# Performance work log

Measured on AMD Instinct MI355X. Metric: run time of the kernel, lower is better.

The kernel has to match this reference:

```python
import jax, jax.numpy as jnp
import numpy as np

IN, H, T = 40, 64, 301


def setup_inputs() -> dict:
    key = jax.random.key(0)
    ks = jax.random.split(key, 7)
    s_ih = 1.0 / np.sqrt(H)
    return {
        "x": jax.random.normal(ks[0], (4096, T, IN), dtype=jnp.float32),
        # PyTorch LSTM layout: gates stacked as [i, f, g, o] along first dim
        "w_ih": jax.random.uniform(ks[1], (4 * H, IN), jnp.float32, -s_ih, s_ih),
        "w_hh": jax.random.uniform(ks[2], (4 * H, H), jnp.float32, -s_ih, s_ih),
        "b_ih": jax.random.uniform(ks[3], (4 * H,), jnp.float32, -s_ih, s_ih),
        "b_hh": jax.random.uniform(ks[4], (4 * H,), jnp.float32, -s_ih, s_ih),
        "w_clf": jax.random.uniform(ks[5], (1, T * H), jnp.float32, -1.0 / np.sqrt(T * H), 1.0 / np.sqrt(T * H)),
        "b_clf": jax.random.uniform(ks[6], (1,), jnp.float32, -1.0 / np.sqrt(T * H), 1.0 / np.sqrt(T * H)),
    }


def _lstm(x, w_ih, w_hh, b_ih, b_hh):
    B = x.shape[0]
    # precompute input projections for all timesteps: [B, T, 4H] -> [T, B, 4H]
    xw = jnp.einsum("bti,gi->btg", x, w_ih) + b_ih + b_hh
    xw = jnp.transpose(xw, (1, 0, 2))

    def step(carry, xt):
        h, c = carry
        z = xt + h @ w_hh.T  # [B, 4H]
        i, f, g, o = jnp.split(z, 4, axis=-1)
        c = jax.nn.sigmoid(f) * c + jax.nn.sigmoid(i) * jnp.tanh(g)
        h = jax.nn.sigmoid(o) * jnp.tanh(c)
        return (h, c), h

    h0 = jnp.zeros((B, H), x.dtype)
    c0 = jnp.zeros((B, H), x.dtype)
    _, hs = jax.lax.scan(step, (h0, c0), xw)  # hs: [T, B, H]
    return jnp.transpose(hs, (1, 0, 2))  # [B, T, H]


def reference(x, w_ih, w_hh, b_ih, b_hh, w_clf, b_clf):
    out = _lstm(x, w_ih, w_hh, b_ih, b_hh)  # [B, T, H]
    flat = out.reshape(out.shape[0], -1)  # [B, T*H]
    return flat @ w_clf.T + b_clf  # [B, 1]
```

## Files before the change

kernel.cpp:

```cpp
#include <hip/hip_runtime.h>

#define T_STEPS 301
#define IN_DIM  40
#define LOG2E   1.44269504088896340736f

typedef __attribute__((ext_vector_type(8))) _Float16 f16x8;
typedef __attribute__((ext_vector_type(4))) float f32x4;
typedef unsigned short ushort_t;
typedef unsigned int uint_t;

union u16cv { _Float16 hf; ushort_t u; };

#define MFMA16(A, B, C) __builtin_amdgcn_mfma_f32_16x16x32_f16((A), (B), (C), 0, 0, 0)

__device__ __forceinline__ f16x8 cvt8h(const float4 a, const float4 b) {
  f16x8 r;
  r[0] = (_Float16)a.x; r[1] = (_Float16)a.y; r[2] = (_Float16)a.z; r[3] = (_Float16)a.w;
  r[4] = (_Float16)b.x; r[5] = (_Float16)b.y; r[6] = (_Float16)b.z; r[7] = (_Float16)b.w;
  return r;
}

__device__ __forceinline__ float lstm_act(float zi, float zf, float zg, float zo, float& cc) {
  const float ig = __builtin_amdgcn_rcpf(1.0f + __builtin_amdgcn_exp2f(-zi));
  const float fg = __builtin_amdgcn_rcpf(1.0f + __builtin_amdgcn_exp2f(-zf));
  const float gg = 1.0f - 2.0f * __builtin_amdgcn_rcpf(1.0f + __builtin_amdgcn_exp2f(zg));
  const float og = __builtin_amdgcn_rcpf(1.0f + __builtin_amdgcn_exp2f(-zo));
  cc = fg * cc + ig * gg;
  const float tc = 1.0f - 2.0f * __builtin_amdgcn_rcpf(1.0f + __builtin_amdgcn_exp2f(cc * (2.0f * LOG2E)));
  return og * tc;
}

__global__ __launch_bounds__(256, 1)
void lstm_fm(const float* __restrict__ x, const float* __restrict__ w_ih,
             const float* __restrict__ w_hh, const float* __restrict__ b_ih,
             const float* __restrict__ b_hh, const float* __restrict__ w_clf,
             const float* __restrict__ b_clf, float* __restrict__ out) {
  extern __shared__ char smem[];
  float*    wclf  = (float*)smem;
  ushort_t* hflat = (ushort_t*)(smem + 77056);
  float*    red   = (float*)(smem + 77056 + 4096);

  const int tid = threadIdx.x;
  const int l   = tid & 63, w = tid >> 6;
  const int c15 = l & 15, g16 = l >> 4;
  const int n   = w * 16 + c15;
  const int b0  = blockIdx.x * 16;
  const float gsc[4] = {LOG2E, LOG2E, 2.0f * LOG2E, LOG2E};

  for (int i = tid; i < (T_STEPS * 64) / 4; i += 256)
    ((float4*)wclf)[i] = ((const float4*)w_clf)[i];
  for (int i = tid; i < 1024; i += 256) ((uint_t*)hflat)[i] = 0;

  f16x8 whh[4][2], wih[4][2];
#pragma unroll
  for (int g = 0; g < 4; ++g) {
    const float s = gsc[g];
    const float* wr = w_hh + (size_t)(g * 64 + n) * 64;
#pragma unroll
    for (int kc = 0; kc < 2; ++kc) {
      float4 v0 = *(const float4*)(wr + kc * 32 + g16 * 8);
      float4 v1 = *(const float4*)(wr + kc * 32 + g16 * 8 + 4);
      v0.x *= s; v0.y *= s; v0.z *= s; v0.w *= s;
      v1.x *= s; v1.y *= s; v1.z *= s; v1.w *= s;
      whh[g][kc] = cvt8h(v0, v1);
    }
    const float* wi = w_ih + (size_t)(g * 64 + n) * IN_DIM;
    {
      float4 v0 = *(const float4*)(wi + g16 * 8);
      float4 v1 = *(const float4*)(wi + g16 * 8 + 4);
      v0.x *= s; v0.y *= s; v0.z *= s; v0.w *= s;
      v1.x *= s; v1.y *= s; v1.z *= s; v1.w *= s;
      wih[g][0] = cvt8h(v0, v1);
    }
    {
      float4 u0 = make_float4(0, 0, 0, 0), u1 = make_float4(0, 0, 0, 0);
      if (g16 == 0) {
        u0 = *(const float4*)(wi + 32);
        u1 = *(const float4*)(wi + 36);
        u0.x *= s; u0.y *= s; u0.z *= s; u0.w *= s;
        u1.x *= s; u1.y *= s; u1.z *= s; u1.w *= s;
      } else if (g16 == 1) {
        u0.x = (b_ih[g * 64 + n] + b_hh[g * 64 + n]) * s;
      }
      wih[g][1] = cvt8h(u0, u1);
    }
  }
  __syncthreads();

  const int akey = (c15 >> 2) << 4;
  const int ridx0 = c15 * 64 + ((0 * 32 + 8 * g16) ^ akey);
  const int ridx1 = c15 * 64 + ((1 * 32 + 8 * g16) ^ akey);
  int widx[4];
#pragma unroll
  for (int r = 0; r < 4; ++r) widx[r] = (4 * g16 + r) * 64 + (n ^ (g16 << 4));

  const float* xb = x + (size_t)(b0 + c15) * T_STEPS * IN_DIM;
  float4 px0 = *(const float4*)(xb + g16 * 8);
  float4 px1 = *(const float4*)(xb + g16 * 8 + 4);
  float4 pq0 = make_float4(0, 0, 0, 0), pq1 = make_float4(0, 0, 0, 0);
  if (g16 == 0) {
    pq0 = *(const float4*)(xb + 32);
    pq1 = *(const float4*)(xb + 36);
  }
  f16x8 xf1c = {};
  if (g16 == 1) xf1c[0] = (_Float16)1.0f;

  f32x4 z[4];
  float cc[4]  = {0.f, 0.f, 0.f, 0.f};
  float acl[4] = {0.f, 0.f, 0.f, 0.f};

  for (int t = 0; t < T_STEPS; ++t) {
    const int rb = (t & 1) * 1024, wb = 1024 - rb;

    f16x8 a0 = *(const f16x8*)(hflat + rb + ridx0);
    f16x8 a1 = *(const f16x8*)(hflat + rb + ridx1);

    f16x8 xf0 = cvt8h(px0, px1);
    f16x8 xf1 = xf1c;
    if (g16 == 0) xf1 = cvt8h(pq0, pq1);
#pragma unroll
    for (int g = 0; g < 4; ++g) {
      f32x4 zz = {0.f, 0.f, 0.f, 0.f};
      zz = MFMA16(xf0, wih[g][0], zz);
      z[g] = MFMA16(xf1, wih[g][1], zz);
    }

    {
      const int tn = (t + 1 < T_STEPS) ? t + 1 : t;
      const float* xp = xb + (size_t)tn * IN_DIM;
      px0 = *(const float4*)(xp + g16 * 8);
      px1 = *(const float4*)(xp + g16 * 8 + 4);
      if (g16 == 0) {
        pq0 = *(const float4*)(xp + 32);
        pq1 = *(const float4*)(xp + 36);
      }
    }

#pragma unroll
    for (int g = 0; g < 4; ++g) {
      z[g] = MFMA16(a0, whh[g][0], z[g]);
      z[g] = MFMA16(a1, whh[g][1], z[g]);
    }

    const float wc = wclf[t * 64 + n];
#pragma unroll
    for (int r = 0; r < 4; ++r) {
      const float h = lstm_act(z[0][r], z[1][r], z[2][r], z[3][r], cc[r]);
      acl[r] += h * wc;
      u16cv cv; cv.hf = (_Float16)h;
      hflat[wb + widx[r]] = cv.u;
    }

    asm volatile("s_waitcnt lgkmcnt(0)\n\ts_barrier" ::: "memory");
  }

#pragma unroll
  for (int m = 1; m <= 8; m <<= 1) {
#pragma unroll
    for (int r = 0; r < 4; ++r) acl[r] += __shfl_xor(acl[r], m);
  }
  if (c15 == 0) {
#pragma unroll
    for (int r = 0; r < 4; ++r) red[w * 16 + 4 * g16 + r] = acl[r];
  }
  __syncthreads();
  if (tid < 16)
    out[b0 + tid] = b_clf[0] + red[tid] + red[16 + tid] + red[32 + tid] + red[48 + tid];
}

extern "C" void kernel_launch(void* const* d_in, const int* in_sizes, int n_in,
                              void* d_out, int out_size, void* d_ws, size_t ws_size,
                              hipStream_t stream) {
  const float* x     = (const float*)d_in[0];
  const float* w_ih  = (const float*)d_in[1];
  const float* w_hh  = (const float*)d_in[2];
  const float* b_ih  = (const float*)d_in[3];
  const float* b_hh  = (const float*)d_in[4];
  const float* w_clf = (const float*)d_in[5];
  const float* b_clf = (const float*)d_in[6];
  float* out = (float*)d_out;

  const size_t shmem = 77056 + 4096 + 256;
  (void)hipFuncSetAttribute((const void*)lstm_fm,
                            hipFuncAttributeMaxDynamicSharedMemorySize, (int)shmem);
  lstm_fm<<<256, 256, shmem, stream>>>(x, w_ih, w_hh, b_ih, b_hh, w_clf, b_clf, out);
}
```

Before: 181.5 us.

## Software-pipeline input projection one step ahead of recurrent MFMA chain

Computes the input-projection MFMAs for step t+1 during step t, with ping-pong accumulators, and prefetches x two steps ahead. The recurrent step then only runs the h·W_hh MFMAs and activations on the critical path, so the x-projection latency overlaps with the LDS read and activation work. The loop is unrolled by two with a peeled final step. This raises register pressure through the second accumulator set.

```diff
diff --git a/kernel.cpp b/kernel.cpp
--- a/kernel.cpp
+++ b/kernel.cpp
@@ -31,7 +31,7 @@
 }
 
 __global__ __launch_bounds__(256, 1)
-void lstm_fm(const float* __restrict__ x, const float* __restrict__ w_ih,
+void lstm_pp(const float* __restrict__ x, const float* __restrict__ w_ih,
              const float* __restrict__ w_hh, const float* __restrict__ b_ih,
              const float* __restrict__ b_hh, const float* __restrict__ w_clf,
              const float* __restrict__ b_clf, float* __restrict__ out) {
@@ -95,64 +95,88 @@
   for (int r = 0; r < 4; ++r) widx[r] = (4 * g16 + r) * 64 + (n ^ (g16 << 4));
 
   const float* xb = x + (size_t)(b0 + c15) * T_STEPS * IN_DIM;
-  float4 px0 = *(const float4*)(xb + g16 * 8);
-  float4 px1 = *(const float4*)(xb + g16 * 8 + 4);
-  float4 pq0 = make_float4(0, 0, 0, 0), pq1 = make_float4(0, 0, 0, 0);
-  if (g16 == 0) {
-    pq0 = *(const float4*)(xb + 32);
-    pq1 = *(const float4*)(xb + 36);
-  }
   f16x8 xf1c = {};
   if (g16 == 1) xf1c[0] = (_Float16)1.0f;
 
-  f32x4 z[4];
+  f32x4 z[4], zn[4];
   float cc[4]  = {0.f, 0.f, 0.f, 0.f};
   float acl[4] = {0.f, 0.f, 0.f, 0.f};
 
-  for (int t = 0; t < T_STEPS; ++t) {
-    const int rb = (t & 1) * 1024, wb = 1024 - rb;
-
-    f16x8 a0 = *(const f16x8*)(hflat + rb + ridx0);
-    f16x8 a1 = *(const f16x8*)(hflat + rb + ridx1);
-
-    f16x8 xf0 = cvt8h(px0, px1);
+  {
+    const float4 v0 = *(const float4*)(xb + g16 * 8);
+    const float4 v1 = *(const float4*)(xb + g16 * 8 + 4);
+    f16x8 xf0 = cvt8h(v0, v1);
     f16x8 xf1 = xf1c;
-    if (g16 == 0) xf1 = cvt8h(pq0, pq1);
+    if (g16 == 0) {
+      const float4 u0 = *(const float4*)(xb + 32);
+      const float4 u1 = *(const float4*)(xb + 36);
+      xf1 = cvt8h(u0, u1);
+    }
 #pragma unroll
     for (int g = 0; g < 4; ++g) {
       f32x4 zz = {0.f, 0.f, 0.f, 0.f};
       zz = MFMA16(xf0, wih[g][0], zz);
       z[g] = MFMA16(xf1, wih[g][1], zz);
     }
-
-    {
-      const int tn = (t + 1 < T_STEPS) ? t + 1 : t;
-      const float* xp = xb + (size_t)tn * IN_DIM;
-      px0 = *(const float4*)(xp + g16 * 8);
-      px1 = *(const float4*)(xp + g16 * 8 + 4);
-      if (g16 == 0) {
-        pq0 = *(const float4*)(xp + 32);
-        pq1 = *(const float4*)(xp + 36);
-      }
-    }
-
-#pragma unroll
-    for (int g = 0; g < 4; ++g) {
-      z[g] = MFMA16(a0, whh[g][0], z[g]);
-      z[g] = MFMA16(a1, whh[g][1], z[g]);
-    }
-
-    const float wc = wclf[t * 64 + n];
-#pragma unroll
-    for (int r = 0; r < 4; ++r) {
-      const float h = lstm_act(z[0][r], z[1][r], z[2][r], z[3][r], cc[r]);
-      acl[r] += h * wc;
-      u16cv cv; cv.hf = (_Float16)h;
-      hflat[wb + widx[r]] = cv.u;
-    }
-
-    asm volatile("s_waitcnt lgkmcnt(0)\n\ts_barrier" ::: "memory");
-  }
+  }
+  float4 px0, px1, pq0 = make_float4(0, 0, 0, 0), pq1 = make_float4(0, 0, 0, 0);
+  {
+    const float* xp = xb + IN_DIM;
+    px0 = *(const float4*)(xp + g16 * 8);
+    px1 = *(const float4*)(xp + g16 * 8 + 4);
+    if (g16 == 0) {
+      pq0 = *(const float4*)(xp + 32);
+      pq1 = *(const float4*)(xp + 36);
+    }
+  }
+
+#define STEP(ZC, ZN, T, LAST)                                                     \
+  {                                                                               \
+    const int rb = ((T) & 1) * 1024, wb = 1024 - rb;                              \
+    f16x8 a0 = *(const f16x8*)(hflat + rb + ridx0);                               \
+    f16x8 a1 = *(const f16x8*)(hflat + rb + ridx1);                               \
+    _Pragma("unroll")                                                             \
+    for (int g = 0; g < 4; ++g) {                                                 \
+      ZC[g] = MFMA16(a0, whh[g][0], ZC[g]);                                       \
+      ZC[g] = MFMA16(a1, whh[g][1], ZC[g]);                                       \
+    }                                                                             \
+    if (!(LAST)) {                                                                \
+      f16x8 xf0 = cvt8h(px0, px1);                                                \
+      f16x8 xf1 = xf1c;                                                           \
+      if (g16 == 0) xf1 = cvt8h(pq0, pq1);                                        \
+      _Pragma("unroll")                                                           \
+      for (int g = 0; g < 4; ++g) {                                               \
+        f32x4 zz = {0.f, 0.f, 0.f, 0.f};                                          \
+        zz = MFMA16(xf0, wih[g][0], zz);                                          \
+        ZN[g] = MFMA16(xf1, wih[g][1], zz);                                       \
+      }                                                                           \
+      const int tn = ((T) + 2 < T_STEPS) ? (T) + 2 : T_STEPS - 1;                 \
+      const float* xp = xb + (size_t)tn * IN_DIM;                                 \
+      px0 = *(const float4*)(xp + g16 * 8);                                       \
+      px1 = *(const float4*)(xp + g16 * 8 + 4);                                   \
+      if (g16 == 0) {                                                             \
+        pq0 = *(const float4*)(xp + 32);                                          \
+        pq1 = *(const float4*)(xp + 36);                                          \
+      }                                                                           \
+    }                                                                             \
+    const float wc = wclf[(T) * 64 + n];                                          \
+    _Pragma("unroll")                                                             \
+    for (int r = 0; r < 4; ++r) {                                                 \
+      const float h = lstm_act(ZC[0][r], ZC[1][r], ZC[2][r], ZC[3][r], cc[r]);    \
+      acl[r] += h * wc;                                                           \
+      u16cv cv; cv.hf = (_Float16)h;                                              \
+      hflat[wb + widx[r]] = cv.u;                                                 \
+    }                                                                             \
+    asm volatile("s_waitcnt lgkmcnt(0)\n\ts_barrier" ::: "memory");               \
+  }
+
+  for (int p = 0; p < 150; ++p) {
+    const int t0 = 2 * p;
+    STEP(z, zn, t0, 0)
+    STEP(zn, z, t0 + 1, 0)
+  }
+  STEP(z, zn, 300, 1)
+#undef STEP
 
 #pragma unroll
   for (int m = 1; m <= 8; m <<= 1) {
@@ -181,7 +205,7 @@
   float* out = (float*)d_out;
 
   const size_t shmem = 77056 + 4096 + 256;
-  (void)hipFuncSetAttribute((const void*)lstm_fm,
+  (void)hipFuncSetAttribute((const void*)lstm_pp,
                             hipFuncAttributeMaxDynamicSharedMemorySize, (int)shmem);
-  lstm_fm<<<256, 256, shmem, stream>>>(x, w_ih, w_hh, b_ih, b_hh, w_clf, b_clf, out);
-}
+  lstm_pp<<<256, 256, shmem, stream>>>(x, w_ih, w_hh, b_ih, b_hh, w_clf, b_clf, out);
+}
```

Measured after the change: 173.6 us, median of 2. 1.05x faster.

## Duplicate each column strip across two waves, splitting activation rows between them

Applied to the files above, without the earlier changes.

Doubles the block to 512 threads (8 waves). Each pair of waves computes the same 16-column gate MFMAs redundantly, but each wave evaluates the nonlinear LSTM activations for only 2 of the 4 accumulator rows, halving the serial transcendental work per wave on the recurrence critical path. Input-projection weights move from registers into LDS and are reloaded every step to relieve register pressure under launch_bounds(512,2). In exchange it adds redundant MFMAs, extra LDS traffic and a barrier spanning more waves.

```diff
diff --git a/kernel.cpp b/kernel.cpp
--- a/kernel.cpp
+++ b/kernel.cpp
@@ -30,28 +30,57 @@
   return og * tc;
 }
 
-__global__ __launch_bounds__(256, 1)
-void lstm_fm(const float* __restrict__ x, const float* __restrict__ w_ih,
+__global__ __launch_bounds__(512, 2)
+void lstm_d2(const float* __restrict__ x, const float* __restrict__ w_ih,
              const float* __restrict__ w_hh, const float* __restrict__ b_ih,
              const float* __restrict__ b_hh, const float* __restrict__ w_clf,
              const float* __restrict__ b_clf, float* __restrict__ out) {
   extern __shared__ char smem[];
   float*    wclf  = (float*)smem;
-  ushort_t* hflat = (ushort_t*)(smem + 77056);
-  float*    red   = (float*)(smem + 77056 + 4096);
+  f16x8*    wihl  = (f16x8*)(smem + 77056);
+  ushort_t* hflat = (ushort_t*)(smem + 77056 + 32768);
+  float*    red   = (float*)(smem + 77056 + 32768 + 4096);
 
   const int tid = threadIdx.x;
-  const int l   = tid & 63, w = tid >> 6;
+  const int l = tid & 63, wv = tid >> 6;
+  const int strip = wv & 3, u = wv >> 2;
   const int c15 = l & 15, g16 = l >> 4;
-  const int n   = w * 16 + c15;
-  const int b0  = blockIdx.x * 16;
+  const int n = strip * 16 + c15;
+  const int b0 = blockIdx.x * 16;
   const float gsc[4] = {LOG2E, LOG2E, 2.0f * LOG2E, LOG2E};
 
-  for (int i = tid; i < (T_STEPS * 64) / 4; i += 256)
+  for (int i = tid; i < (T_STEPS * 64) / 4; i += 512)
     ((float4*)wclf)[i] = ((const float4*)w_clf)[i];
-  for (int i = tid; i < 1024; i += 256) ((uint_t*)hflat)[i] = 0;
-
-  f16x8 whh[4][2], wih[4][2];
+  for (int i = tid; i < 1024; i += 512) ((uint_t*)hflat)[i] = 0;
+  if (tid < 128) red[tid] = 0.f;
+
+  for (int idx = tid; idx < 2048; idx += 512) {
+    const int l2 = idx & 63;
+    const int kc = (idx >> 6) & 1;
+    const int g  = (idx >> 7) & 3;
+    const int st = idx >> 9;
+    const int nn = st * 16 + (l2 & 15);
+    const int kg = l2 >> 4;
+    const float s = gsc[g];
+    const float* wi = w_ih + (size_t)(g * 64 + nn) * IN_DIM;
+    float4 v0 = make_float4(0, 0, 0, 0), v1 = make_float4(0, 0, 0, 0);
+    if (kc == 0) {
+      v0 = *(const float4*)(wi + kg * 8);
+      v1 = *(const float4*)(wi + kg * 8 + 4);
+      v0.x *= s; v0.y *= s; v0.z *= s; v0.w *= s;
+      v1.x *= s; v1.y *= s; v1.z *= s; v1.w *= s;
+    } else if (kg == 0) {
+      v0 = *(const float4*)(wi + 32);
+      v1 = *(const float4*)(wi + 36);
+      v0.x *= s; v0.y *= s; v0.z *= s; v0.w *= s;
+      v1.x *= s; v1.y *= s; v1.z *= s; v1.w *= s;
+    } else if (kg == 1) {
+      v0.x = (b_ih[g * 64 + nn] + b_hh[g * 64 + nn]) * s;
+    }
+    wihl[idx] = cvt8h(v0, v1);
+  }
+
+  f16x8 whh[4][2];
 #pragma unroll
   for (int g = 0; g < 4; ++g) {
     const float s = gsc[g];
@@ -64,35 +93,16 @@
       v1.x *= s; v1.y *= s; v1.z *= s; v1.w *= s;
       whh[g][kc] = cvt8h(v0, v1);
     }
-    const float* wi = w_ih + (size_t)(g * 64 + n) * IN_DIM;
-    {
-      float4 v0 = *(const float4*)(wi + g16 * 8);
-      float4 v1 = *(const float4*)(wi + g16 * 8 + 4);
-      v0.x *= s; v0.y *= s; v0.z *= s; v0.w *= s;
-      v1.x *= s; v1.y *= s; v1.z *= s; v1.w *= s;
-      wih[g][0] = cvt8h(v0, v1);
-    }
-    {
-      float4 u0 = make_float4(0, 0, 0, 0), u1 = make_float4(0, 0, 0, 0);
-      if (g16 == 0) {
-        u0 = *(const float4*)(wi + 32);
-        u1 = *(const float4*)(wi + 36);
-        u0.x *= s; u0.y *= s; u0.z *= s; u0.w *= s;
-        u1.x *= s; u1.y *= s; u1.z *= s; u1.w *= s;
-      } else if (g16 == 1) {
-        u0.x = (b_ih[g * 64 + n] + b_hh[g * 64 + n]) * s;
-      }
-      wih[g][1] = cvt8h(u0, u1);
-    }
   }
   __syncthreads();
 
   const int akey = (c15 >> 2) << 4;
-  const int ridx0 = c15 * 64 + ((0 * 32 + 8 * g16) ^ akey);
-  const int ridx1 = c15 * 64 + ((1 * 32 + 8 * g16) ^ akey);
-  int widx[4];
-#pragma unroll
-  for (int r = 0; r < 4; ++r) widx[r] = (4 * g16 + r) * 64 + (n ^ (g16 << 4));
+  const int ridx0 = c15 * 64 + ((8 * g16) ^ akey);
+  const int ridx1 = c15 * 64 + ((32 + 8 * g16) ^ akey);
+  const int r0 = 2 * u, r1 = 2 * u + 1;
+  const int widx0 = (4 * g16 + r0) * 64 + (n ^ (g16 << 4));
+  const int widx1 = (4 * g16 + r1) * 64 + (n ^ (g16 << 4));
+  const f16x8* const wbase = &wihl[(strip * 4) * 2 * 64 + l];
 
   const float* xb = x + (size_t)(b0 + c15) * T_STEPS * IN_DIM;
   float4 px0 = *(const float4*)(xb + g16 * 8);
@@ -106,11 +116,10 @@
   if (g16 == 1) xf1c[0] = (_Float16)1.0f;
 
   f32x4 z[4];
-  float cc[4]  = {0.f, 0.f, 0.f, 0.f};
-  float acl[4] = {0.f, 0.f, 0.f, 0.f};
+  float cc0 = 0.f, cc1 = 0.f, acl0 = 0.f, acl1 = 0.f;
 
   for (int t = 0; t < T_STEPS; ++t) {
-    const int rb = (t & 1) * 1024, wb = 1024 - rb;
+    const int rb = (t & 1) * 1024, wb2 = 1024 - rb;
 
     f16x8 a0 = *(const f16x8*)(hflat + rb + ridx0);
     f16x8 a1 = *(const f16x8*)(hflat + rb + ridx1);
@@ -120,9 +129,11 @@
     if (g16 == 0) xf1 = cvt8h(pq0, pq1);
 #pragma unroll
     for (int g = 0; g < 4; ++g) {
+      const f16x8 w0 = wbase[(g * 2 + 0) * 64];
+      const f16x8 w1 = wbase[(g * 2 + 1) * 64];
       f32x4 zz = {0.f, 0.f, 0.f, 0.f};
-      zz = MFMA16(xf0, wih[g][0], zz);
-      z[g] = MFMA16(xf1, wih[g][1], zz);
+      zz = MFMA16(xf0, w0, zz);
+      z[g] = MFMA16(xf1, w1, zz);
     }
 
     {
@@ -143,29 +154,41 @@
     }
 
     const float wc = wclf[t * 64 + n];
-#pragma unroll
-    for (int r = 0; r < 4; ++r) {
-      const float h = lstm_act(z[0][r], z[1][r], z[2][r], z[3][r], cc[r]);
-      acl[r] += h * wc;
-      u16cv cv; cv.hf = (_Float16)h;
-      hflat[wb + widx[r]] = cv.u;
-    }
+    float h0, h1;
+    if (u == 0) {
+      h0 = lstm_act(z[0][0], z[1][0], z[2][0], z[3][0], cc0);
+      h1 = lstm_act(z[0][1], z[1][1], z[2][1], z[3][1], cc1);
+    } else {
+      h0 = lstm_act(z[0][2], z[1][2], z[2][2], z[3][2], cc0);
+      h1 = lstm_act(z[0][3], z[1][3], z[2][3], z[3][3], cc1);
+    }
+    acl0 += h0 * wc;
+    acl1 += h1 * wc;
+    u16cv cv0, cv1;
+    cv0.hf = (_Float16)h0;
+    cv1.hf = (_Float16)h1;
+    hflat[wb2 + widx0] = cv0.u;
+    hflat[wb2 + widx1] = cv1.u;
 
     asm volatile("s_waitcnt lgkmcnt(0)\n\ts_barrier" ::: "memory");
   }
 
 #pragma unroll
   for (int m = 1; m <= 8; m <<= 1) {
-#pragma unroll
-    for (int r = 0; r < 4; ++r) acl[r] += __shfl_xor(acl[r], m);
+    acl0 += __shfl_xor(acl0, m);
+    acl1 += __shfl_xor(acl1, m);
   }
   if (c15 == 0) {
-#pragma unroll
-    for (int r = 0; r < 4; ++r) red[w * 16 + 4 * g16 + r] = acl[r];
+    red[wv * 16 + 4 * g16 + r0] = acl0;
+    red[wv * 16 + 4 * g16 + r1] = acl1;
   }
   __syncthreads();
-  if (tid < 16)
-    out[b0 + tid] = b_clf[0] + red[tid] + red[16 + tid] + red[32 + tid] + red[48 + tid];
+  if (tid < 16) {
+    float s = b_clf[0];
+#pragma unroll
+    for (int w2 = 0; w2 < 8; ++w2) s += red[w2 * 16 + tid];
+    out[b0 + tid] = s;
+  }
 }
 
 extern "C" void kernel_launch(void* const* d_in, const int* in_sizes, int n_in,
@@ -180,8 +203,8 @@
   const float* b_clf = (const float*)d_in[6];
   float* out = (float*)d_out;
 
-  const size_t shmem = 77056 + 4096 + 256;
-  (void)hipFuncSetAttribute((const void*)lstm_fm,
+  const size_t shmem = 77056 + 32768 + 4096 + 512;
+  (void)hipFuncSetAttribute((const void*)lstm_d2,
                             hipFuncAttributeMaxDynamicSharedMemorySize, (int)shmem);
-  lstm_fm<<<256, 256, shmem, stream>>>(x, w_ih, w_hh, b_ih, b_hh, w_clf, b_clf, out);
-}
+  lstm_d2<<<256, 512, shmem, stream>>>(x, w_ih, w_hh, b_ih, b_hh, w_clf, b_clf, out);
+}
```

After: 276.0 us. 1.52x slower.

## Split batch tile into two interleaved groups and pack two timesteps per MFMA

Applied to the files above, without the earlier changes.

Restructures the recurrence so each 16-row MFMA tile holds 8 batch rows for two consecutive timesteps. The x projection for step t+1 is computed together with step t and carried in the spare accumulator rows, so the odd step only issues the recurrent h·W_hh MFMAs. Two independent batch halves (A and B) are interleaved to give the scheduler parallel dependency chains, and each half has its own shared-memory h buffer. The cost is more registers and extra LDS, plus more complex indexing.

```diff
diff --git a/kernel.cpp b/kernel.cpp
--- a/kernel.cpp
+++ b/kernel.cpp
@@ -31,14 +31,15 @@
 }
 
 __global__ __launch_bounds__(256, 1)
-void lstm_fm(const float* __restrict__ x, const float* __restrict__ w_ih,
+void lstm_dg(const float* __restrict__ x, const float* __restrict__ w_ih,
              const float* __restrict__ w_hh, const float* __restrict__ b_ih,
              const float* __restrict__ b_hh, const float* __restrict__ w_clf,
              const float* __restrict__ b_clf, float* __restrict__ out) {
   extern __shared__ char smem[];
-  float*    wclf  = (float*)smem;
-  ushort_t* hflat = (ushort_t*)(smem + 77056);
-  float*    red   = (float*)(smem + 77056 + 4096);
+  float*    wclf = (float*)smem;
+  ushort_t* hA   = (ushort_t*)(smem + 77056);
+  ushort_t* hB   = (ushort_t*)(smem + 77056 + 4096);
+  float*    red  = (float*)(smem + 77056 + 8192);
 
   const int tid = threadIdx.x;
   const int l   = tid & 63, w = tid >> 6;
@@ -49,7 +50,7 @@
 
   for (int i = tid; i < (T_STEPS * 64) / 4; i += 256)
     ((float4*)wclf)[i] = ((const float4*)w_clf)[i];
-  for (int i = tid; i < 1024; i += 256) ((uint_t*)hflat)[i] = 0;
+  for (int i = tid; i < 2048; i += 256) ((uint_t*)hA)[i] = 0;
 
   f16x8 whh[4][2], wih[4][2];
 #pragma unroll
@@ -87,81 +88,167 @@
   }
   __syncthreads();
 
-  const int akey = (c15 >> 2) << 4;
-  const int ridx0 = c15 * 64 + ((0 * 32 + 8 * g16) ^ akey);
-  const int ridx1 = c15 * 64 + ((1 * 32 + 8 * g16) ^ akey);
-  int widx[4];
-#pragma unroll
-  for (int r = 0; r < 4; ++r) widx[r] = (4 * g16 + r) * 64 + (n ^ (g16 << 4));
-
-  const float* xb = x + (size_t)(b0 + c15) * T_STEPS * IN_DIM;
-  float4 px0 = *(const float4*)(xb + g16 * 8);
-  float4 px1 = *(const float4*)(xb + g16 * 8 + 4);
-  float4 pq0 = make_float4(0, 0, 0, 0), pq1 = make_float4(0, 0, 0, 0);
+  const int toff = (c15 >> 1) & 1;
+  const int sx   = 2 * (c15 >> 2) + (c15 & 1);
+  const float* xbA = x + (size_t)(b0 + sx) * T_STEPS * IN_DIM;
+  const float* xbB = x + (size_t)(b0 + 8 + sx) * T_STEPS * IN_DIM;
+
+  const int akey  = (c15 >> 2) << 4;
+  const int ridx0 = c15 * 64 + ((8 * g16) ^ akey);
+  const int ridx1 = c15 * 64 + ((32 + 8 * g16) ^ akey);
+  const int widx0 = (4 * g16) * 64 + (n ^ (g16 << 4));
+  const int widx1 = (4 * g16 + 1) * 64 + (n ^ (g16 << 4));
+
+  float4 pA0 = *(const float4*)(xbA + toff * IN_DIM + g16 * 8);
+  float4 pA1 = *(const float4*)(xbA + toff * IN_DIM + g16 * 8 + 4);
+  float4 qA0 = make_float4(0, 0, 0, 0), qA1 = make_float4(0, 0, 0, 0);
+  float4 pB0 = *(const float4*)(xbB + toff * IN_DIM + g16 * 8);
+  float4 pB1 = *(const float4*)(xbB + toff * IN_DIM + g16 * 8 + 4);
+  float4 qB0 = make_float4(0, 0, 0, 0), qB1 = make_float4(0, 0, 0, 0);
   if (g16 == 0) {
-    pq0 = *(const float4*)(xb + 32);
-    pq1 = *(const float4*)(xb + 36);
+    qA0 = *(const float4*)(xbA + toff * IN_DIM + 32);
+    qA1 = *(const float4*)(xbA + toff * IN_DIM + 36);
+    qB0 = *(const float4*)(xbB + toff * IN_DIM + 32);
+    qB1 = *(const float4*)(xbB + toff * IN_DIM + 36);
   }
   f16x8 xf1c = {};
   if (g16 == 1) xf1c[0] = (_Float16)1.0f;
 
-  f32x4 z[4];
-  float cc[4]  = {0.f, 0.f, 0.f, 0.f};
-  float acl[4] = {0.f, 0.f, 0.f, 0.f};
-
-  for (int t = 0; t < T_STEPS; ++t) {
-    const int rb = (t & 1) * 1024, wb = 1024 - rb;
-
-    f16x8 a0 = *(const f16x8*)(hflat + rb + ridx0);
-    f16x8 a1 = *(const f16x8*)(hflat + rb + ridx1);
-
-    f16x8 xf0 = cvt8h(px0, px1);
-    f16x8 xf1 = xf1c;
-    if (g16 == 0) xf1 = cvt8h(pq0, pq1);
-#pragma unroll
-    for (int g = 0; g < 4; ++g) {
-      f32x4 zz = {0.f, 0.f, 0.f, 0.f};
-      zz = MFMA16(xf0, wih[g][0], zz);
-      z[g] = MFMA16(xf1, wih[g][1], zz);
-    }
-
-    {
-      const int tn = (t + 1 < T_STEPS) ? t + 1 : t;
-      const float* xp = xb + (size_t)tn * IN_DIM;
-      px0 = *(const float4*)(xp + g16 * 8);
-      px1 = *(const float4*)(xp + g16 * 8 + 4);
-      if (g16 == 0) {
-        pq0 = *(const float4*)(xp + 32);
-        pq1 = *(const float4*)(xp + 36);
-      }
-    }
-
-#pragma unroll
-    for (int g = 0; g < 4; ++g) {
-      z[g] = MFMA16(a0, whh[g][0], z[g]);
-      z[g] = MFMA16(a1, whh[g][1], z[g]);
-    }
-
-    const float wc = wclf[t * 64 + n];
-#pragma unroll
-    for (int r = 0; r < 4; ++r) {
-      const float h = lstm_act(z[0][r], z[1][r], z[2][r], z[3][r], cc[r]);
-      acl[r] += h * wc;
-      u16cv cv; cv.hf = (_Float16)h;
-      hflat[wb + widx[r]] = cv.u;
-    }
-
-    asm volatile("s_waitcnt lgkmcnt(0)\n\ts_barrier" ::: "memory");
+  f32x4 zA[4], zB[4];
+  float ccA0 = 0.f, ccA1 = 0.f, ccB0 = 0.f, ccB1 = 0.f;
+  float aclA0 = 0.f, aclA1 = 0.f, aclB0 = 0.f, aclB1 = 0.f;
+
+  for (int p = 0; p < 151; ++p) {
+    const int t0 = 2 * p;
+    {
+      f16x8 aA0 = *(const f16x8*)(hA + ridx0);
+      f16x8 aA1 = *(const f16x8*)(hA + ridx1);
+      f16x8 aB0 = *(const f16x8*)(hB + ridx0);
+      f16x8 aB1 = *(const f16x8*)(hB + ridx1);
+
+      const f16x8 xA0 = cvt8h(pA0, pA1);
+      const f16x8 xA1 = (g16 == 0) ? cvt8h(qA0, qA1) : xf1c;
+      const f16x8 xB0 = cvt8h(pB0, pB1);
+      const f16x8 xB1 = (g16 == 0) ? cvt8h(qB0, qB1) : xf1c;
+#pragma unroll
+      for (int g = 0; g < 4; ++g) {
+        f32x4 zz = {0.f, 0.f, 0.f, 0.f};
+        zz = MFMA16(xA0, wih[g][0], zz);
+        zA[g] = MFMA16(xA1, wih[g][1], zz);
+      }
+#pragma unroll
+      for (int g = 0; g < 4; ++g) {
+        zA[g] = MFMA16(aA0, whh[g][0], zA[g]);
+        zA[g] = MFMA16(aA1, whh[g][1], zA[g]);
+      }
+#pragma unroll
+      for (int g = 0; g < 4; ++g) {
+        f32x4 zz = {0.f, 0.f, 0.f, 0.f};
+        zz = MFMA16(xB0, wih[g][0], zz);
+        zB[g] = MFMA16(xB1, wih[g][1], zz);
+      }
+#pragma unroll
+      for (int g = 0; g < 4; ++g) {
+        zB[g] = MFMA16(aB0, whh[g][0], zB[g]);
+        zB[g] = MFMA16(aB1, whh[g][1], zB[g]);
+      }
+
+      {
+        const int tq = t0 + 2 + toff;
+        const int tm = (tq <= T_STEPS - 1) ? tq : T_STEPS - 1;
+        pA0 = *(const float4*)(xbA + (size_t)tm * IN_DIM + g16 * 8);
+        pA1 = *(const float4*)(xbA + (size_t)tm * IN_DIM + g16 * 8 + 4);
+        pB0 = *(const float4*)(xbB + (size_t)tm * IN_DIM + g16 * 8);
+        pB1 = *(const float4*)(xbB + (size_t)tm * IN_DIM + g16 * 8 + 4);
+        if (g16 == 0) {
+          qA0 = *(const float4*)(xbA + (size_t)tm * IN_DIM + 32);
+          qA1 = *(const float4*)(xbA + (size_t)tm * IN_DIM + 36);
+          qB0 = *(const float4*)(xbB + (size_t)tm * IN_DIM + 32);
+          qB1 = *(const float4*)(xbB + (size_t)tm * IN_DIM + 36);
+        }
+      }
+
+      const float wc = wclf[t0 * 64 + n];
+      {
+        const float h = lstm_act(zA[0][0], zA[1][0], zA[2][0], zA[3][0], ccA0);
+        aclA0 += h * wc;
+        u16cv cv; cv.hf = (_Float16)h; hA[1024 + widx0] = cv.u;
+      }
+      {
+        const float h = lstm_act(zA[0][1], zA[1][1], zA[2][1], zA[3][1], ccA1);
+        aclA1 += h * wc;
+        u16cv cv; cv.hf = (_Float16)h; hA[1024 + widx1] = cv.u;
+      }
+      {
+        const float h = lstm_act(zB[0][0], zB[1][0], zB[2][0], zB[3][0], ccB0);
+        aclB0 += h * wc;
+        u16cv cv; cv.hf = (_Float16)h; hB[1024 + widx0] = cv.u;
+      }
+      {
+        const float h = lstm_act(zB[0][1], zB[1][1], zB[2][1], zB[3][1], ccB1);
+        aclB1 += h * wc;
+        u16cv cv; cv.hf = (_Float16)h; hB[1024 + widx1] = cv.u;
+      }
+      if (p == 150) break;
+      asm volatile("s_waitcnt lgkmcnt(0)\n\ts_barrier" ::: "memory");
+    }
+    {
+      f16x8 aA0 = *(const f16x8*)(hA + 1024 + ridx0);
+      f16x8 aA1 = *(const f16x8*)(hA + 1024 + ridx1);
+      f16x8 aB0 = *(const f16x8*)(hB + 1024 + ridx0);
+      f16x8 aB1 = *(const f16x8*)(hB + 1024 + ridx1);
+
+      f32x4 sA[4], sB[4];
+#pragma unroll
+      for (int g = 0; g < 4; ++g) {
+        sA[g] = __builtin_shufflevector(zA[g], zA[g], 2, 3, 2, 3);
+        sA[g] = MFMA16(aA0, whh[g][0], sA[g]);
+        sA[g] = MFMA16(aA1, whh[g][1], sA[g]);
+      }
+#pragma unroll
+      for (int g = 0; g < 4; ++g) {
+        sB[g] = __builtin_shufflevector(zB[g], zB[g], 2, 3, 2, 3);
+        sB[g] = MFMA16(aB0, whh[g][0], sB[g]);
+        sB[g] = MFMA16(aB1, whh[g][1], sB[g]);
+      }
+
+      const float wc = wclf[(t0 + 1) * 64 + n];
+      {
+        const float h = lstm_act(sA[0][0], sA[1][0], sA[2][0], sA[3][0], ccA0);
+        aclA0 += h * wc;
+        u16cv cv; cv.hf = (_Float16)h; hA[widx0] = cv.u;
+      }
+      {
+        const float h = lstm_act(sA[0][1], sA[1][1], sA[2][1], sA[3][1], ccA1);
+        aclA1 += h * wc;
+        u16cv cv; cv.hf = (_Float16)h; hA[widx1] = cv.u;
+      }
+      {
+        const float h = lstm_act(sB[0][0], sB[1][0], sB[2][0], sB[3][0], ccB0);
+        aclB0 += h * wc;
+        u16cv cv; cv.hf = (_Float16)h; hB[widx0] = cv.u;
+      }
+      {
+        const float h = lstm_act(sB[0][1], sB[1][1], sB[2][1], sB[3][1], ccB1);
+        aclB1 += h * wc;
+        u16cv cv; cv.hf = (_Float16)h; hB[widx1] = cv.u;
+      }
+      asm volatile("s_waitcnt lgkmcnt(0)\n\ts_barrier" ::: "memory");
+    }
   }
 
 #pragma unroll
   for (int m = 1; m <= 8; m <<= 1) {
-#pragma unroll
-    for (int r = 0; r < 4; ++r) acl[r] += __shfl_xor(acl[r], m);
+    aclA0 += __shfl_xor(aclA0, m);
+    aclA1 += __shfl_xor(aclA1, m);
+    aclB0 += __shfl_xor(aclB0, m);
+    aclB1 += __shfl_xor(aclB1, m);
   }
   if (c15 == 0) {
-#pragma unroll
-    for (int r = 0; r < 4; ++r) red[w * 16 + 4 * g16 + r] = acl[r];
+    red[w * 16 + 2 * g16]         = aclA0;
+    red[w * 16 + 2 * g16 + 1]     = aclA1;
+    red[w * 16 + 8 + 2 * g16]     = aclB0;
+    red[w * 16 + 8 + 2 * g16 + 1] = aclB1;
   }
   __syncthreads();
   if (tid < 16)
@@ -180,8 +267,8 @@
   const float* b_clf = (const float*)d_in[6];
   float* out = (float*)d_out;
 
-  const size_t shmem = 77056 + 4096 + 256;
-  (void)hipFuncSetAttribute((const void*)lstm_fm,
+  const size_t shmem = 77056 + 4096 + 4096 + 256;
+  (void)hipFuncSetAttribute((const void*)lstm_dg,
                             hipFuncAttributeMaxDynamicSharedMemorySize, (int)shmem);
-  lstm_fm<<<256, 256, shmem, stream>>>(x, w_ih, w_hh, b_ih, b_hh, w_clf, b_clf, out);
-}
+  lstm_dg<<<256, 256, shmem, stream>>>(x, w_ih, w_hh, b_ih, b_hh, w_clf, b_clf, out);
+}
```

Measured after the change: 229.1 us. 26.2% more time.
